# Kernel optimization log

Hardware: AMD Instinct MI355X
Metric: run time of the kernel (lower is better)

Reference implementation:

```python
import jax, jax.numpy as jnp
import numpy as np

N = 30000   # nodes
E = 600000  # edges (avg degree 20)
H = 128     # hidden_channels
L = 4       # num_layers
G = 64      # graphs in batch


def _init(key, shape, fan_in):
    return (jax.random.normal(key, shape, jnp.float32) / np.sqrt(fan_in)).astype(jnp.float32)


def setup_inputs() -> dict:
    key = jax.random.key(0)
    ks = jax.random.split(key, 24)
    x = jax.random.normal(ks[0], (N, 1), jnp.float32)
    pos = jax.random.normal(ks[1], (N, 3), jnp.float32)
    edge_index = jax.random.randint(ks[2], (2, E), 0, N, dtype=jnp.int32).astype(jnp.int64)
    batch = jnp.sort(jax.random.randint(ks[3], (N,), 0, G, dtype=jnp.int32)).astype(jnp.int64)

    emb_w = _init(ks[4], (1, H), 1)
    emb_b = jnp.zeros((H,), jnp.float32)

    # stacked per-layer params: msg MLP (2H+1 -> H -> H), node MLP (2H -> H -> H)
    msg_w1 = _init(ks[5], (L, 2 * H + 1, H), 2 * H + 1)
    msg_b1 = jnp.zeros((L, H), jnp.float32)
    msg_w2 = _init(ks[6], (L, H, H), H)
    msg_b2 = jnp.zeros((L, H), jnp.float32)
    node_w1 = _init(ks[7], (L, 2 * H, H), 2 * H)
    node_b1 = jnp.zeros((L, H), jnp.float32)
    node_w2 = _init(ks[8], (L, H, H), H)
    node_b2 = jnp.zeros((L, H), jnp.float32)

    out_w1 = _init(ks[9], (H, 32), H)
    out_b1 = jnp.zeros((32,), jnp.float32)
    out_w2 = _init(ks[10], (32, 1), 32)
    out_b2 = jnp.zeros((1,), jnp.float32)

    return {
        "x": x, "pos": pos, "edge_index": edge_index, "batch": batch,
        "emb_w": emb_w, "emb_b": emb_b,
        "msg_w1": msg_w1, "msg_b1": msg_b1, "msg_w2": msg_w2, "msg_b2": msg_b2,
        "node_w1": node_w1, "node_b1": node_b1, "node_w2": node_w2, "node_b2": node_b2,
        "out_w1": out_w1, "out_b1": out_b1, "out_w2": out_w2, "out_b2": out_b2,
    }


def reference(x, pos, edge_index, batch,
              emb_w, emb_b,
              msg_w1, msg_b1, msg_w2, msg_b2,
              node_w1, node_b1, node_w2, node_b2,
              out_w1, out_b1, out_w2, out_b2):
    row, col = edge_index[0], edge_index[1]  # row = source j, col = target i
    # edge scalar: squared distance (computed once, reused across layers)
    dist_sq = jnp.sum((pos[row] - pos[col]) ** 2, axis=-1, keepdims=True)  # [E,1]

    h = x @ emb_w + emb_b  # [N,H]
    for l in range(L):
        x_j = h[row]   # source features
        x_i = h[col]   # target features
        m = jnp.concatenate([x_i, x_j, dist_sq], axis=-1)           # [E, 2H+1]
        m = jax.nn.silu(m @ msg_w1[l] + msg_b1[l]) @ msg_w2[l] + msg_b2[l]  # [E,H]
        aggr = jax.ops.segment_sum(m, col, num_segments=N)          # scatter-add to targets
        nh = jnp.concatenate([h, aggr], axis=-1)                    # [N, 2H]
        h = jax.nn.silu(nh @ node_w1[l] + node_b1[l]) @ node_w2[l] + node_b2[l]
        # dropout omitted for deterministic reference (eval mode)

    g = jax.ops.segment_sum(h, batch, num_segments=G)               # global_add_pool [G,H]
    return jax.nn.silu(g @ out_w1 + out_b1) @ out_w2 + out_b2       # [G,1]
```

## Files before the change

kernel.cpp:

```cpp
#include <hip/hip_runtime.h>

typedef unsigned short u16;
typedef __bf16 bf16x8 __attribute__((ext_vector_type(8)));
typedef float f32x4 __attribute__((ext_vector_type(4)));

#define HN 128
#define TM 64
#define LTM 16
#define ASTRIDE 136

__device__ __forceinline__ u16 f2bf(float f) {
  union { float f; unsigned u; } v; v.f = f;
  unsigned r = v.u + 0x7fffu + ((v.u >> 16) & 1u);
  return (u16)(r >> 16);
}
__device__ __forceinline__ float bf2f(u16 v) {
  union { unsigned u; float f; } x; x.u = ((unsigned)v) << 16; return x.f;
}
__device__ __forceinline__ float bflo(unsigned v) {
  union { unsigned u; float f; } x; x.u = v << 16; return x.f;
}
__device__ __forceinline__ float bfhi(unsigned v) {
  union { unsigned u; float f; } x; x.u = v & 0xffff0000u; return x.f;
}
__device__ __forceinline__ float silu_f(float x) {
  float e = __builtin_amdgcn_exp2f(-1.442695041f * x);
  return x * __builtin_amdgcn_rcpf(1.f + e);
}

__global__ void pack_weights(const float* __restrict__ msg_w1, const float* __restrict__ msg_w2,
                             const float* __restrict__ node_w1, const float* __restrict__ node_w2,
                             u16* __restrict__ pw, int* __restrict__ deg,
                             float* __restrict__ g, int N_, int GH) {
  int id = blockIdx.x * 256 + threadIdx.x;
  if (id < N_) deg[id] = 0;
  if (id < GH) g[id] = 0.f;
  if (id >= 4 * 6 * 16384) return;
  int l = id / (6 * 16384);
  int rem = id % (6 * 16384);
  int m = rem / 16384;
  int e = rem % 16384;
  int kg = e >> 10;
  int n = (e >> 3) & 127;
  int j = e & 7;
  int k = kg * 8 + j;
  float v = 0.f;
  switch (m) {
    case 0: v = msg_w1[(l * 257 + k) * 128 + n]; break;
    case 1: v = msg_w1[(l * 257 + 128 + k) * 128 + n]; break;
    case 2: v = msg_w2[(l * 128 + k) * 128 + n]; break;
    case 3: v = node_w1[(l * 256 + k) * 128 + n]; break;
    case 4: v = node_w1[(l * 256 + 128 + k) * 128 + n]; break;
    case 5: v = node_w2[(l * 128 + k) * 128 + n]; break;
  }
  pw[id] = f2bf(v);
}

__device__ __forceinline__ void gemm64(const u16* s_A, const u16* s_W,
                                       int w, int quad, int m16, f32x4 acc[8]) {
#pragma unroll
  for (int ks = 0; ks < 4; ks++) {
    bf16x8 a = *(const bf16x8*)&s_A[(w * 16 + m16) * ASTRIDE + ks * 32 + quad * 8];
#pragma unroll
    for (int ct = 0; ct < 8; ct++) {
      bf16x8 b = *(const bf16x8*)&s_W[(ks * 4 + quad) * 1024 + (ct * 16 + m16) * 8];
      acc[ct] = __builtin_amdgcn_mfma_f32_16x16x32_bf16(a, b, acc[ct], 0, 0, 0);
    }
  }
}

__device__ __forceinline__ void gemm16_gb(const u16* s_A, const u16* __restrict__ gW,
                                          int ch, int quad, int m16, f32x4 acc[2]) {
#pragma unroll
  for (int ks = 0; ks < 4; ks++) {
    bf16x8 a = *(const bf16x8*)&s_A[m16 * ASTRIDE + ks * 32 + quad * 8];
#pragma unroll
    for (int ct = 0; ct < 2; ct++) {
      bf16x8 b = *(const bf16x8*)&gW[(ks * 4 + quad) * 1024 + ((ch * 2 + ct) * 16 + m16) * 8];
      acc[ct] = __builtin_amdgcn_mfma_f32_16x16x32_bf16(a, b, acc[ct], 0, 0, 0);
    }
  }
}

__device__ __forceinline__ void gemm16_ra_gb(const bf16x8 aH[4], const u16* __restrict__ gW,
                                             int ch, int quad, int m16, f32x4 acc[2]) {
#pragma unroll
  for (int ks = 0; ks < 4; ks++) {
#pragma unroll
    for (int ct = 0; ct < 2; ct++) {
      bf16x8 b = *(const bf16x8*)&gW[(ks * 4 + quad) * 1024 + ((ch * 2 + ct) * 16 + m16) * 8];
      acc[ct] = __builtin_amdgcn_mfma_f32_16x16x32_bf16(aH[ks], b, acc[ct], 0, 0, 0);
    }
  }
}

__global__ __launch_bounds__(256) void fold_kernel(
    const float* __restrict__ msg_w2, const float* __restrict__ node_w1,
    const float* __restrict__ msg_b2, const u16* __restrict__ pw,
    u16* __restrict__ pwc, float* __restrict__ vc,
    const float* __restrict__ msg_w1, const float* __restrict__ emb_w,
    const float* __restrict__ emb_b, const float* __restrict__ msg_b1,
    float* __restrict__ uv) {
  __shared__ __align__(16) u16 s_A[TM * ASTRIDE];
  __shared__ __align__(16) u16 s_W[16384];
  const int t = threadIdx.x;
  const int w = t >> 6, lane = t & 63, quad = lane >> 4, m16 = lane & 15;
  const int b = blockIdx.x, l = b >> 1, half = b & 1;
  const int tile0 = half * 64;

  {
    int r = t >> 2, qo = (t & 3) * 32;
    const float4* src = (const float4*)(msg_w2 + (size_t)(l * 128 + tile0 + r) * 128 + qo);
    u16* dst = s_A + r * ASTRIDE + qo;
#pragma unroll
    for (int i = 0; i < 8; i++) {
      float4 v = src[i];
      ushort4 o;
      o.x = f2bf(v.x); o.y = f2bf(v.y); o.z = f2bf(v.z); o.w = f2bf(v.w);
      *(ushort4*)(dst + i * 4) = o;
    }
  }
  {
    const int4* src = (const int4*)(pw + (size_t)(l * 6 + 4) * 16384);
    int4* dst = (int4*)s_W;
#pragma unroll
    for (int i = 0; i < 8; i++) dst[t + i * 256] = src[t + i * 256];
  }
  __syncthreads();
  f32x4 acc[8];
#pragma unroll
  for (int ct = 0; ct < 8; ct++) acc[ct] = {0.f, 0.f, 0.f, 0.f};
  gemm64(s_A, s_W, w, quad, m16, acc);
#pragma unroll
  for (int ct = 0; ct < 8; ct++)
#pragma unroll
    for (int j = 0; j < 4; j++) {
      int k = tile0 + w * 16 + quad * 4 + j;
      int n = ct * 16 + m16;
      pwc[(size_t)l * 16384 + (k >> 3) * 1024 + n * 8 + (k & 7)] = f2bf(acc[ct][j]);
    }
  if (half == 0 && t < 128) {
    float s = 0.f;
    for (int np = 0; np < 128; np++)
      s += msg_b2[l * 128 + np] * node_w1[(size_t)(l * 256 + 128 + np) * 128 + t];
    vc[l * 128 + t] = s;
  }
  if (l == 0 && half == 1 && t < 128) {
    float up = 0.f, vp = 0.f, uq = 0.f, vq = 0.f;
    for (int k = 0; k < 128; k++) {
      float wa = msg_w1[(size_t)k * 128 + t];
      float wb = msg_w1[(size_t)(128 + k) * 128 + t];
      up = fmaf(emb_w[k], wa, up);
      vp = fmaf(emb_b[k], wa, vp);
      uq = fmaf(emb_w[k], wb, uq);
      vq = fmaf(emb_b[k], wb, vq);
    }
    uv[t] = up;
    uv[128 + t] = vp + vq + msg_b1[t];
    uv[256 + t] = uq;
  }
}

__global__ void hist_kernel(const int* __restrict__ eidx, int* __restrict__ deg,
                            int* __restrict__ rnk, int E_) {
  int e = blockIdx.x * 256 + threadIdx.x;
  if (e < E_) rnk[e] = atomicAdd(&deg[eidx[E_ + e]], 1);
}

__global__ void scan1_kernel(const int* __restrict__ deg, int* __restrict__ off,
                             int* __restrict__ bsum, int n) {
  __shared__ int s[256];
  int t = threadIdx.x;
  int i = blockIdx.x * 256 + t;
  int v = (i < n) ? deg[i] : 0;
  s[t] = v;
  for (int d = 1; d < 256; d <<= 1) {
    __syncthreads();
    int x = (t >= d) ? s[t - d] : 0;
    __syncthreads();
    s[t] += x;
  }
  __syncthreads();
  if (i < n) off[i] = s[t] - v;
  if (t == 255) bsum[blockIdx.x] = s[255];
}

__global__ void scan2_kernel(int* __restrict__ bsum, int nb) {
  __shared__ int s[256];
  int t = threadIdx.x;
  int v = (t < nb) ? bsum[t] : 0;
  s[t] = v;
  for (int d = 1; d < 256; d <<= 1) {
    __syncthreads();
    int x = (t >= d) ? s[t - d] : 0;
    __syncthreads();
    s[t] += x;
  }
  __syncthreads();
  if (t < nb) bsum[t] = s[t] - v;
}

__global__ void scan3_kernel(int* __restrict__ off, const int* __restrict__ bsum, int n) {
  int i = blockIdx.x * 256 + threadIdx.x;
  if (i < n) off[i] += bsum[blockIdx.x];
}

__global__ void scatter_kernel(const int* __restrict__ eidx, const float* __restrict__ pos,
                               const int* __restrict__ off, const int* __restrict__ rnk,
                               int2* __restrict__ es8, int E_) {
  int e = blockIdx.x * 256 + threadIdx.x;
  if (e >= E_) return;
  int sr = eidx[e], tg = eidx[E_ + e];
  float dx = pos[sr * 3 + 0] - pos[tg * 3 + 0];
  float dy = pos[sr * 3 + 1] - pos[tg * 3 + 1];
  float dz = pos[sr * 3 + 2] - pos[tg * 3 + 2];
  float d = dx * dx + dy * dy + dz * dz;
  int p = off[tg] + rnk[e];
  int2 v;
  v.x = sr | (tg << 15);
  v.y = __float_as_int(d);
  es8[p] = v;
}

__device__ __forceinline__ void edge_step_lds(
    int tg_s, float dd_s, unsigned qv,
    int& cur_s, float& p0, float& p1, float& s0, float& s1,
    const u16* __restrict__ P, float* s_S, int cp,
    float wd0, float wd1, int tile0) {
  if (tg_s != cur_s) {
    if (cur_s >= 0) {
      float* dst = &s_S[(cur_s - tile0) * HN + cp];
      atomicAdd(dst, s0);
      atomicAdd(dst + 1, s1);
    }
    cur_s = tg_s; s0 = 0.f; s1 = 0.f;
    int cg = tg_s < 0 ? 0 : tg_s;
    unsigned pv = *(const unsigned*)&P[(size_t)cg * HN + cp];
    p0 = bflo(pv); p1 = bfhi(pv);
  }
  float x0 = p0 + bflo(qv) + dd_s * wd0;
  float x1 = p1 + bfhi(qv) + dd_s * wd1;
  s0 += silu_f(x0);
  s1 += silu_f(x1);
}

__device__ __forceinline__ void edge_step_r1(
    int tg_s, float dd_s, float xs,
    int& cur_s, float& p0, float& p1, float& s0, float& s1,
    const float* s_xt, float* s_S, int cp,
    float wd0, float wd1, float uP0, float uP1, float vP0, float vP1,
    float uQ0, float uQ1, int tile0) {
  if (tg_s != cur_s) {
    if (cur_s >= 0) {
      float* dst = &s_S[(cur_s - tile0) * HN + cp];
      atomicAdd(dst, s0);
      atomicAdd(dst + 1, s1);
    }
    cur_s = tg_s; s0 = 0.f; s1 = 0.f;
    int ci = tg_s < 0 ? 0 : (tg_s - tile0);
    float xt = s_xt[ci];
    p0 = fmaf(xt, uP0, vP0);
    p1 = fmaf(xt, uP1, vP1);
  }
  float x0 = fmaf(dd_s, wd0, fmaf(xs, uQ0, p0));
  float x1 = fmaf(dd_s, wd1, fmaf(xs, uQ1, p1));
  s0 += silu_f(x0);
  s1 += silu_f(x1);
}

template <bool FUSE, bool RANK1>
__global__ __launch_bounds__(256) void layer_kernel(
    const u16* __restrict__ P, const u16* __restrict__ Q,
    const u16* __restrict__ hbf, u16* __restrict__ hout,
    const int* __restrict__ off, const int* __restrict__ deg,
    const float* __restrict__ w1d, const int2* __restrict__ es8,
    const u16* __restrict__ pwc, const float* __restrict__ vc,
    const u16* __restrict__ pwn, const float* __restrict__ b1, const float* __restrict__ b2,
    const u16* __restrict__ pw_next, const float* __restrict__ b1_next,
    u16* __restrict__ Pout, u16* __restrict__ Qout,
    const float* __restrict__ xin, const float* __restrict__ uv,
    const float* __restrict__ emb_w, const float* __restrict__ emb_b,
    int nnodes, int E_) {
  __shared__ float s_S[LTM * HN];
  __shared__ __align__(16) u16 s_A[LTM * ASTRIDE];
  __shared__ float s_xt[LTM];
  const int t = threadIdx.x;
  const int w = t >> 6, lane = t & 63, quad = lane >> 4, m16 = lane & 15;
  const int tile0 = blockIdx.x * LTM;
  const int ch = w;

  {
    float4 z = {0.f, 0.f, 0.f, 0.f};
    float4* p4 = (float4*)s_S;
#pragma unroll
    for (int i = 0; i < 2; i++) p4[t + i * 256] = z;
  }
  if constexpr (RANK1) {
    if (t < LTM) {
      int n = tile0 + t;
      s_xt[t] = (n < nnodes) ? xin[n] : 0.f;
    }
  }
  __syncthreads();

  const int cp = lane * 2;
  const float2 wdv = *(const float2*)&w1d[cp];
  const float wd0 = wdv.x, wd1 = wdv.y;
  const int e_lo = off[tile0];
  const int e_hi = (tile0 + LTM < nnodes) ? off[tile0 + LTM] : E_;
  const int span = e_hi - e_lo;
  const int wstart = e_lo + (span * w) / 4;
  const int wend = e_lo + (span * (w + 1)) / 4;
  const int total = wend - wstart;
  const int nchunks = (total + 63) >> 6;

  int cur_s = -1;
  float s0 = 0.f, s1 = 0.f, p0 = 0.f, p1 = 0.f;

  if constexpr (RANK1) {
    __shared__ float s_xs[4][2][64];
    const float uP0 = uv[cp], uP1 = uv[cp + 1];
    const float vP0 = uv[128 + cp], vP1 = uv[128 + cp + 1];
    const float uQ0 = uv[256 + cp], uQ1 = uv[256 + cp + 1];
    if (nchunks > 0) {
      int2* ebuf = (int2*)(s_A + (w * 4) * ASTRIDE);
      float* xsb = &s_xs[w][0][0];
      {
        int e = wstart + lane;
        int2 v;
        if (e < wend) v = es8[e];
        else { v.x = (int)0xFFFF8000; v.y = 0; }
        float xl = xin[v.x & 0x7fff];
        ebuf[lane] = v;
        xsb[lane] = xl;
      }
      asm volatile("s_waitcnt lgkmcnt(0)" ::: "memory");
      int tg[8]; float dd[8]; float xs[8];
#pragma unroll
      for (int j = 0; j < 8; j++) {
        int2 v = ebuf[j];
        tg[j] = v.x >> 15; dd[j] = __int_as_float(v.y);
        xs[j] = xsb[j];
      }

      for (int ci = 0; ci < nchunks; ci++) {
        const int cs = (ci & 1), ns = ((ci + 1) & 1);
        const int2* cb = ebuf + cs * 64;
        const float* cx = xsb + cs * 64;
        const int2* nb = ebuf + ns * 64;
        const float* nx = xsb + ns * 64;
        int2 vnext; vnext.x = (int)0xFFFF8000; vnext.y = 0;
        {
          int e = wstart + (ci + 1) * 64 + lane;
          if (ci + 1 < nchunks && e < wend) vnext = es8[e];
        }
#pragma unroll
        for (int g = 0; g < 3; g++) {
          int tgn[8]; float ddn[8]; float xsn[8];
#pragma unroll
          for (int j = 0; j < 8; j++) {
            int2 v = cb[(g + 1) * 8 + j];
            tgn[j] = v.x >> 15; ddn[j] = __int_as_float(v.y);
            xsn[j] = cx[(g + 1) * 8 + j];
          }
#pragma unroll
          for (int j = 0; j < 8; j++) {
            int tg_s = __builtin_amdgcn_readfirstlane(tg[j]);
            edge_step_r1(tg_s, dd[j], xs[j], cur_s, p0, p1, s0, s1, s_xt, s_S, cp,
                         wd0, wd1, uP0, uP1, vP0, vP1, uQ0, uQ1, tile0);
          }
#pragma unroll
          for (int j = 0; j < 8; j++) { tg[j] = tgn[j]; dd[j] = ddn[j]; xs[j] = xsn[j]; }
        }
        float xnext = xin[vnext.x & 0x7fff];
#pragma unroll
        for (int g = 3; g < 7; g++) {
          int tgn[8]; float ddn[8]; float xsn[8];
#pragma unroll
          for (int j = 0; j < 8; j++) {
            int2 v = cb[(g + 1) * 8 + j];
            tgn[j] = v.x >> 15; ddn[j] = __int_as_float(v.y);
            xsn[j] = cx[(g + 1) * 8 + j];
          }
#pragma unroll
          for (int j = 0; j < 8; j++) {
            int tg_s = __builtin_amdgcn_readfirstlane(tg[j]);
            edge_step_r1(tg_s, dd[j], xs[j], cur_s, p0, p1, s0, s1, s_xt, s_S, cp,
                         wd0, wd1, uP0, uP1, vP0, vP1, uQ0, uQ1, tile0);
          }
#pragma unroll
          for (int j = 0; j < 8; j++) { tg[j] = tgn[j]; dd[j] = ddn[j]; xs[j] = xsn[j]; }
        }
        ebuf[ns * 64 + lane] = vnext;
        xsb[ns * 64 + lane] = xnext;
        asm volatile("s_waitcnt lgkmcnt(0)" ::: "memory");
        {
          int tgn[8]; float ddn[8]; float xsn[8];
#pragma unroll
          for (int j = 0; j < 8; j++) {
            int2 v = nb[j];
            tgn[j] = v.x >> 15; ddn[j] = __int_as_float(v.y);
            xsn[j] = nx[j];
          }
#pragma unroll
          for (int j = 0; j < 8; j++) {
            int tg_s = __builtin_amdgcn_readfirstlane(tg[j]);
            edge_step_r1(tg_s, dd[j], xs[j], cur_s, p0, p1, s0, s1, s_xt, s_S, cp,
                         wd0, wd1, uP0, uP1, vP0, vP1, uQ0, uQ1, tile0);
          }
#pragma unroll
          for (int j = 0; j < 8; j++) { tg[j] = tgn[j]; dd[j] = ddn[j]; xs[j] = xsn[j]; }
        }
      }
      if (cur_s >= 0) {
        float* dst = &s_S[(cur_s - tile0) * HN + cp];
        atomicAdd(dst, s0);
        atomicAdd(dst + 1, s1);
      }
    }
  } else {
    if (nchunks > 0) {
      int2* ebuf = (int2*)(s_A + (w * 4) * ASTRIDE);
      {
        int e = wstart + lane;
        int2 v;
        if (e < wend) v = es8[e];
        else { v.x = (int)0xFFFF8000; v.y = 0; }
        ebuf[lane] = v;
      }
      asm volatile("s_waitcnt lgkmcnt(0)" ::: "memory");
      int tg[8]; float dd[8]; unsigned qv[8];
#pragma unroll
      for (int j = 0; j < 8; j++) {
        int2 v = ebuf[j];
        tg[j] = v.x >> 15; dd[j] = __int_as_float(v.y);
        qv[j] = *(const unsigned*)&Q[(size_t)(v.x & 0x7fff) * HN + cp];
      }

      for (int ci = 0; ci < nchunks; ci++) {
        const int2* cb = ebuf + (ci & 1) * 64;
        const int2* nb = ebuf + ((ci + 1) & 1) * 64;
        int2 vnext; vnext.x = (int)0xFFFF8000; vnext.y = 0;
        {
          int e = wstart + (ci + 1) * 64 + lane;
          if (ci + 1 < nchunks && e < wend) vnext = es8[e];
        }
#pragma unroll
        for (int g = 0; g < 7; g++) {
          int tgn[8]; float ddn[8]; unsigned qvn[8];
#pragma unroll
          for (int j = 0; j < 8; j++) {
            int2 v = cb[(g + 1) * 8 + j];
            tgn[j] = v.x >> 15; ddn[j] = __int_as_float(v.y);
            qvn[j] = *(const unsigned*)&Q[(size_t)(v.x & 0x7fff) * HN + cp];
          }
#pragma unroll
          for (int j = 0; j < 8; j++) {
            int tg_s = __builtin_amdgcn_readfirstlane(tg[j]);
            edge_step_lds(tg_s, dd[j], qv[j], cur_s, p0, p1, s0, s1, P, s_S, cp, wd0, wd1, tile0);
          }
#pragma unroll
          for (int j = 0; j < 8; j++) { tg[j] = tgn[j]; dd[j] = ddn[j]; qv[j] = qvn[j]; }
        }
        ebuf[((ci + 1) & 1) * 64 + lane] = vnext;
        asm volatile("s_waitcnt lgkmcnt(0)" ::: "memory");
        {
          int tgn[8]; float ddn[8]; unsigned qvn[8];
#pragma unroll
          for (int j = 0; j < 8; j++) {
            int2 v = nb[j];
            tgn[j] = v.x >> 15; ddn[j] = __int_as_float(v.y);
            qvn[j] = *(const unsigned*)&Q[(size_t)(v.x & 0x7fff) * HN + cp];
          }
#pragma unroll
          for (int j = 0; j < 8; j++) {
            int tg_s = __builtin_amdgcn_readfirstlane(tg[j]);
            edge_step_lds(tg_s, dd[j], qv[j], cur_s, p0, p1, s0, s1, P, s_S, cp, wd0, wd1, tile0);
          }
#pragma unroll
          for (int j = 0; j < 8; j++) { tg[j] = tgn[j]; dd[j] = ddn[j]; qv[j] = qvn[j]; }
        }
      }
      if (cur_s >= 0) {
        float* dst = &s_S[(cur_s - tile0) * HN + cp];
        atomicAdd(dst, s0);
        atomicAdd(dst + 1, s1);
      }
    }
  }
  __syncthreads();

  {
    int srow = w * 4 + (lane >> 4);
    int scol = (lane & 15) * 8;
    const float4* src = (const float4*)&s_S[srow * HN + scol];
    u16* dst = s_A + srow * ASTRIDE + scol;
    float4 v0 = src[0];
    float4 v1 = src[1];
    ushort4 o0, o1;
    o0.x = f2bf(v0.x); o0.y = f2bf(v0.y); o0.z = f2bf(v0.z); o0.w = f2bf(v0.w);
    o1.x = f2bf(v1.x); o1.y = f2bf(v1.y); o1.z = f2bf(v1.z); o1.w = f2bf(v1.w);
    *(ushort4*)(dst + 0) = o0;
    *(ushort4*)(dst + 4) = o1;
  }
  __syncthreads();

  float bb1[2], vcr[2], bb2[2], bbn[2];
#pragma unroll
  for (int ct = 0; ct < 2; ct++) {
    int c = (ch * 2 + ct) * 16 + m16;
    bb1[ct] = b1[c];
    vcr[ct] = vc[c];
    bb2[ct] = b2[c];
    bbn[ct] = FUSE ? b1_next[c] : 0.f;
  }
  int nodem = tile0 + m16;
  if (nodem >= nnodes) nodem = nnodes - 1;

  f32x4 acc[2];
#pragma unroll
  for (int ct = 0; ct < 2; ct++) acc[ct] = {0.f, 0.f, 0.f, 0.f};
  gemm16_gb(s_A, pwc, ch, quad, m16, acc);

  bf16x8 aH[4];
  if constexpr (RANK1) {
    float xv = s_xt[m16];
#pragma unroll
    for (int ks = 0; ks < 4; ks++) {
      u16 hv[8];
#pragma unroll
      for (int i = 0; i < 8; i++) {
        int c = ks * 32 + quad * 8 + i;
        hv[i] = f2bf(fmaf(xv, emb_w[c], emb_b[c]));
      }
      aH[ks] = *(bf16x8*)hv;
    }
  } else {
#pragma unroll
    for (int ks = 0; ks < 4; ks++)
      aH[ks] = *(const bf16x8*)&hbf[(size_t)nodem * HN + ks * 32 + quad * 8];
  }
  gemm16_ra_gb(aH, pwn, ch, quad, m16, acc);

  {
    float degv[4];
#pragma unroll
    for (int j = 0; j < 4; j++) {
      int n = tile0 + quad * 4 + j;
      if (n >= nnodes) n = nnodes - 1;
      degv[j] = (float)deg[n];
    }
#pragma unroll
    for (int ct = 0; ct < 2; ct++)
#pragma unroll
      for (int j = 0; j < 4; j++) {
        int row = quad * 4 + j;
        float xv = acc[ct][j] + bb1[ct] + degv[j] * vcr[ct];
        s_A[row * ASTRIDE + (ch * 2 + ct) * 16 + m16] = f2bf(silu_f(xv));
      }
  }
  __syncthreads();

#pragma unroll
  for (int ct = 0; ct < 2; ct++) acc[ct] = {0.f, 0.f, 0.f, 0.f};
  gemm16_gb(s_A, pwn + 32768, ch, quad, m16, acc);

#pragma unroll
  for (int ct = 0; ct < 2; ct++)
#pragma unroll
    for (int j = 0; j < 4; j++) {
      int row = quad * 4 + j;
      int n = tile0 + row;
      u16 hv = f2bf(acc[ct][j] + bb2[ct]);
      if (n < nnodes) hout[(size_t)n * HN + (ch * 2 + ct) * 16 + m16] = hv;
      if (FUSE) s_A[row * ASTRIDE + (ch * 2 + ct) * 16 + m16] = hv;
    }

  if (FUSE) {
    __syncthreads();
#pragma unroll
    for (int ct = 0; ct < 2; ct++) acc[ct] = {0.f, 0.f, 0.f, 0.f};
    gemm16_gb(s_A, pw_next, ch, quad, m16, acc);
#pragma unroll
    for (int ct = 0; ct < 2; ct++)
#pragma unroll
      for (int j = 0; j < 4; j++) {
        int n = tile0 + quad * 4 + j;
        if (n < nnodes) Pout[(size_t)n * HN + (ch * 2 + ct) * 16 + m16] = f2bf(acc[ct][j] + bbn[ct]);
      }
#pragma unroll
    for (int ct = 0; ct < 2; ct++) acc[ct] = {0.f, 0.f, 0.f, 0.f};
    gemm16_gb(s_A, pw_next + 16384, ch, quad, m16, acc);
#pragma unroll
    for (int ct = 0; ct < 2; ct++)
#pragma unroll
      for (int j = 0; j < 4; j++) {
        int n = tile0 + quad * 4 + j;
        if (n < nnodes) Qout[(size_t)n * HN + (ch * 2 + ct) * 16 + m16] = f2bf(acc[ct][j]);
      }
  }
}

__global__ __launch_bounds__(256) void pool_kernel(
    const u16* __restrict__ h, const int* __restrict__ batch,
    float* __restrict__ g, int N) {
  __shared__ int s_b[64];
  const int t = threadIdx.x;
  const int n0 = blockIdx.x * 64;
  if (t < 64) {
    int n = n0 + t;
    s_b[t] = (n < N) ? batch[n] : -1;
  }
  __syncthreads();
  const int cp = (t & 63) * 2;
  const int rg = t >> 6;
  int cur = -1;
  float s0 = 0.f, s1 = 0.f;
#pragma unroll 4
  for (int i = 0; i < 16; i++) {
    int r = rg * 16 + i;
    int b = s_b[r];
    if (b < 0) break;
    if (b != cur) {
      if (cur >= 0) {
        atomicAdd(&g[cur * HN + cp], s0);
        atomicAdd(&g[cur * HN + cp + 1], s1);
      }
      cur = b; s0 = 0.f; s1 = 0.f;
    }
    unsigned v = *(const unsigned*)&h[(size_t)(n0 + r) * HN + cp];
    s0 += bf2f((u16)(v & 0xffffu));
    s1 += bf2f((u16)(v >> 16));
  }
  if (cur >= 0) {
    atomicAdd(&g[cur * HN + cp], s0);
    atomicAdd(&g[cur * HN + cp + 1], s1);
  }
}

__global__ __launch_bounds__(64) void out_kernel(
    const float* __restrict__ g, const float* __restrict__ w1,
    const float* __restrict__ b1, const float* __restrict__ w2,
    const float* __restrict__ b2, float* __restrict__ out) {
  const int gi = blockIdx.x;
  const int t = threadIdx.x;
  const int c = t & 31, kh = t >> 5;
  float s = 0.f;
  for (int k = kh * 64; k < kh * 64 + 64; k++)
    s += g[gi * HN + k] * w1[k * 32 + c];
  s += __shfl_down(s, 32);
  float r = 0.f;
  if (kh == 0) r = silu_f(s + b1[c]) * w2[c];
  r += __shfl_down(r, 16);
  r += __shfl_down(r, 8);
  r += __shfl_down(r, 4);
  r += __shfl_down(r, 2);
  r += __shfl_down(r, 1);
  if (t == 0) out[gi] = r + b2[0];
}

extern "C" void kernel_launch(void* const* d_in, const int* in_sizes, int n_in,
                              void* d_out, int out_size, void* d_ws, size_t ws_size,
                              hipStream_t stream) {
  const float* x = (const float*)d_in[0];
  const float* pos = (const float*)d_in[1];
  const int* eidx = (const int*)d_in[2];
  const int* batch = (const int*)d_in[3];
  const float* emb_w = (const float*)d_in[4];
  const float* emb_b = (const float*)d_in[5];
  const float* msg_w1 = (const float*)d_in[6];
  const float* msg_b1 = (const float*)d_in[7];
  const float* msg_w2 = (const float*)d_in[8];
  const float* msg_b2 = (const float*)d_in[9];
  const float* node_w1 = (const float*)d_in[10];
  const float* node_b1 = (const float*)d_in[11];
  const float* node_w2 = (const float*)d_in[12];
  const float* node_b2 = (const float*)d_in[13];
  const float* out_w1 = (const float*)d_in[14];
  const float* out_b1 = (const float*)d_in[15];
  const float* out_w2 = (const float*)d_in[16];
  const float* out_b2 = (const float*)d_in[17];
  float* outp = (float*)d_out;

  const int N = 30000, E = 600000, G = 64;
  const size_t NH = (size_t)N * HN;

  u16* hA = (u16*)d_ws;
  u16* hB = hA + NH;
  u16* Pa = hB + NH;
  u16* Qa = Pa + NH;
  u16* Pb = Qa + NH;
  u16* Qb = Pb + NH;
  int2* es8 = (int2*)(Qb + NH);
  int* deg = (int*)(es8 + E);
  int* off = deg + N;
  int* bsum = off + N;
  float* g = (float*)(bsum + 128);
  u16* pw = (u16*)(g + G * HN);
  u16* pwc = pw + (size_t)4 * 6 * 16384;
  float* vcb = (float*)(pwc + (size_t)4 * 16384);
  float* uvb = vcb + 4 * 128;
  int* rnk = (int*)Pb;

  const int NB = (N + 255) / 256;
  const int NLB = (N + LTM - 1) / LTM;

  pack_weights<<<(4 * 6 * 16384 + 255) / 256, 256, 0, stream>>>(
      msg_w1, msg_w2, node_w1, node_w2, pw, deg, g, N, G * HN);
  fold_kernel<<<8, 256, 0, stream>>>(msg_w2, node_w1, msg_b2, pw, pwc, vcb,
                                     msg_w1, emb_w, emb_b, msg_b1, uvb);

  hist_kernel<<<(E + 255) / 256, 256, 0, stream>>>(eidx, deg, rnk, E);
  scan1_kernel<<<NB, 256, 0, stream>>>(deg, off, bsum, N);
  scan2_kernel<<<1, 256, 0, stream>>>(bsum, NB);
  scan3_kernel<<<NB, 256, 0, stream>>>(off, bsum, N);
  scatter_kernel<<<(E + 255) / 256, 256, 0, stream>>>(eidx, pos, off, rnk, es8, E);


  for (int l = 0; l < 4; l++) {
    const u16* pwl = pw + (size_t)(l * 6) * 16384;
    const float* w1d = msg_w1 + (size_t)(l * 257 + 256) * 128;
    u16* hin = (l & 1) ? hA : hB;
    u16* hot = (l & 1) ? hB : hA;
    u16* Pin = (l & 1) ? Pb : Pa;
    u16* Qin = (l & 1) ? Qb : Qa;
    u16* Pot = (l & 1) ? Pa : Pb;
    u16* Qot = (l & 1) ? Qa : Qb;
    if (l == 0) {
      layer_kernel<true, true><<<NLB, 256, 0, stream>>>(
          Pin, Qin, hin, hot, off, deg, w1d, es8,
          pwc + (size_t)l * 16384, vcb + l * 128,
          pwl + 3 * 16384, node_b1 + l * 128, node_b2 + l * 128,
          pw + (size_t)((l + 1) * 6) * 16384, msg_b1 + (l + 1) * 128, Pot, Qot,
          x, uvb, emb_w, emb_b, N, E);
    } else if (l < 3) {
      layer_kernel<true, false><<<NLB, 256, 0, stream>>>(
          Pin, Qin, hin, hot, off, deg, w1d, es8,
          pwc + (size_t)l * 16384, vcb + l * 128,
          pwl + 3 * 16384, node_b1 + l * 128, node_b2 + l * 128,
          pw + (size_t)((l + 1) * 6) * 16384, msg_b1 + (l + 1) * 128, Pot, Qot,
          x, uvb, emb_w, emb_b, N, E);
    } else {
      layer_kernel<false, false><<<NLB, 256, 0, stream>>>(
          Pin, Qin, hin, hot, off, deg, w1d, es8,
          pwc + (size_t)l * 16384, vcb + l * 128,
          pwl + 3 * 16384, node_b1 + l * 128, node_b2 + l * 128,
          nullptr, nullptr, nullptr, nullptr,
          x, uvb, emb_w, emb_b, N, E);
    }
  }

  pool_kernel<<<(N + 63) / 64, 256, 0, stream>>>(hB, batch, g, N);
  out_kernel<<<G, 64, 0, stream>>>(g, out_w1, out_b1, out_w2, out_b2, outp);
}
```

Before: 411.6 us.

## Double layer-kernel node tile to 32 rows with 512-thread blocks

Raises the per-block node tile from 16 to 32 nodes and doubles block size to 8 waves. Edge ranges are split across 8 waves, and the node-MLP GEMMs assign each wave a 16-row half and a 32-column chunk, so weights fetched from global memory are reused across twice as many rows. Padding edges (negative target) now return early instead of being clamped. Larger blocks halve the grid and may lower occupancy. NLB is not shown changing with LTM, so grid sizing must already derive from it.

```diff
diff --git a/kernel.cpp b/kernel.cpp
--- a/kernel.cpp
+++ b/kernel.cpp
@@ -6,7 +6,7 @@
 
 #define HN 128
 #define TM 64
-#define LTM 16
+#define LTM 32
 #define ASTRIDE 136
 
 __device__ __forceinline__ u16 f2bf(float f) {
@@ -69,11 +69,11 @@
   }
 }
 
-__device__ __forceinline__ void gemm16_gb(const u16* s_A, const u16* __restrict__ gW,
-                                          int ch, int quad, int m16, f32x4 acc[2]) {
+__device__ __forceinline__ void gemm32q_gb(const u16* s_A, const u16* __restrict__ gW,
+                                           int rh, int ch, int quad, int m16, f32x4 acc[2]) {
 #pragma unroll
   for (int ks = 0; ks < 4; ks++) {
-    bf16x8 a = *(const bf16x8*)&s_A[m16 * ASTRIDE + ks * 32 + quad * 8];
+    bf16x8 a = *(const bf16x8*)&s_A[(rh * 16 + m16) * ASTRIDE + ks * 32 + quad * 8];
 #pragma unroll
     for (int ct = 0; ct < 2; ct++) {
       bf16x8 b = *(const bf16x8*)&gW[(ks * 4 + quad) * 1024 + ((ch * 2 + ct) * 16 + m16) * 8];
@@ -82,8 +82,8 @@
   }
 }
 
-__device__ __forceinline__ void gemm16_ra_gb(const bf16x8 aH[4], const u16* __restrict__ gW,
-                                             int ch, int quad, int m16, f32x4 acc[2]) {
+__device__ __forceinline__ void gemm32q_ra_gb(const bf16x8 aH[4], const u16* __restrict__ gW,
+                                              int ch, int quad, int m16, f32x4 acc[2]) {
 #pragma unroll
   for (int ks = 0; ks < 4; ks++) {
 #pragma unroll
@@ -227,6 +227,7 @@
     int& cur_s, float& p0, float& p1, float& s0, float& s1,
     const u16* __restrict__ P, float* s_S, int cp,
     float wd0, float wd1, int tile0) {
+  if (tg_s < 0) return;
   if (tg_s != cur_s) {
     if (cur_s >= 0) {
       float* dst = &s_S[(cur_s - tile0) * HN + cp];
@@ -234,8 +235,7 @@
       atomicAdd(dst + 1, s1);
     }
     cur_s = tg_s; s0 = 0.f; s1 = 0.f;
-    int cg = tg_s < 0 ? 0 : tg_s;
-    unsigned pv = *(const unsigned*)&P[(size_t)cg * HN + cp];
+    unsigned pv = *(const unsigned*)&P[(size_t)tg_s * HN + cp];
     p0 = bflo(pv); p1 = bfhi(pv);
   }
   float x0 = p0 + bflo(qv) + dd_s * wd0;
@@ -250,6 +250,7 @@
     const float* s_xt, float* s_S, int cp,
     float wd0, float wd1, float uP0, float uP1, float vP0, float vP1,
     float uQ0, float uQ1, int tile0) {
+  if (tg_s < 0) return;
   if (tg_s != cur_s) {
     if (cur_s >= 0) {
       float* dst = &s_S[(cur_s - tile0) * HN + cp];
@@ -257,8 +258,7 @@
       atomicAdd(dst + 1, s1);
     }
     cur_s = tg_s; s0 = 0.f; s1 = 0.f;
-    int ci = tg_s < 0 ? 0 : (tg_s - tile0);
-    float xt = s_xt[ci];
+    float xt = s_xt[tg_s - tile0];
     p0 = fmaf(xt, uP0, vP0);
     p1 = fmaf(xt, uP1, vP1);
   }
@@ -269,7 +269,7 @@
 }
 
 template <bool FUSE, bool RANK1>
-__global__ __launch_bounds__(256) void layer_kernel(
+__global__ __launch_bounds__(512) void layer_kernel(
     const u16* __restrict__ P, const u16* __restrict__ Q,
     const u16* __restrict__ hbf, u16* __restrict__ hout,
     const int* __restrict__ off, const int* __restrict__ deg,
@@ -287,13 +287,14 @@
   const int t = threadIdx.x;
   const int w = t >> 6, lane = t & 63, quad = lane >> 4, m16 = lane & 15;
   const int tile0 = blockIdx.x * LTM;
-  const int ch = w;
+  const int rh = w >> 2;
+  const int ch = w & 3;
 
   {
     float4 z = {0.f, 0.f, 0.f, 0.f};
     float4* p4 = (float4*)s_S;
 #pragma unroll
-    for (int i = 0; i < 2; i++) p4[t + i * 256] = z;
+    for (int i = 0; i < 2; i++) p4[t + i * 512] = z;
   }
   if constexpr (RANK1) {
     if (t < LTM) {
@@ -309,8 +310,8 @@
   const int e_lo = off[tile0];
   const int e_hi = (tile0 + LTM < nnodes) ? off[tile0 + LTM] : E_;
   const int span = e_hi - e_lo;
-  const int wstart = e_lo + (span * w) / 4;
-  const int wend = e_lo + (span * (w + 1)) / 4;
+  const int wstart = e_lo + (span * w) / 8;
+  const int wend = e_lo + (span * (w + 1)) / 8;
   const int total = wend - wstart;
   const int nchunks = (total + 63) >> 6;
 
@@ -318,7 +319,7 @@
   float s0 = 0.f, s1 = 0.f, p0 = 0.f, p1 = 0.f;
 
   if constexpr (RANK1) {
-    __shared__ float s_xs[4][2][64];
+    __shared__ float s_xs[8][2][64];
     const float uP0 = uv[cp], uP1 = uv[cp + 1];
     const float vP0 = uv[128 + cp], vP1 = uv[128 + cp + 1];
     const float uQ0 = uv[256 + cp], uQ1 = uv[256 + cp + 1];
@@ -514,17 +515,17 @@
     bb2[ct] = b2[c];
     bbn[ct] = FUSE ? b1_next[c] : 0.f;
   }
-  int nodem = tile0 + m16;
+  int nodem = tile0 + rh * 16 + m16;
   if (nodem >= nnodes) nodem = nnodes - 1;
 
   f32x4 acc[2];
 #pragma unroll
   for (int ct = 0; ct < 2; ct++) acc[ct] = {0.f, 0.f, 0.f, 0.f};
-  gemm16_gb(s_A, pwc, ch, quad, m16, acc);
+  gemm32q_gb(s_A, pwc, rh, ch, quad, m16, acc);
 
   bf16x8 aH[4];
   if constexpr (RANK1) {
-    float xv = s_xt[m16];
+    float xv = s_xt[rh * 16 + m16];
 #pragma unroll
     for (int ks = 0; ks < 4; ks++) {
       u16 hv[8];
@@ -540,13 +541,13 @@
     for (int ks = 0; ks < 4; ks++)
       aH[ks] = *(const bf16x8*)&hbf[(size_t)nodem * HN + ks * 32 + quad * 8];
   }
-  gemm16_ra_gb(aH, pwn, ch, quad, m16, acc);
+  gemm32q_ra_gb(aH, pwn, ch, quad, m16, acc);
 
   {
     float degv[4];
 #pragma unroll
     for (int j = 0; j < 4; j++) {
-      int n = tile0 + quad * 4 + j;
+      int n = tile0 + rh * 16 + quad * 4 + j;
       if (n >= nnodes) n = nnodes - 1;
       degv[j] = (float)deg[n];
     }
@@ -554,7 +555,7 @@
     for (int ct = 0; ct < 2; ct++)
 #pragma unroll
       for (int j = 0; j < 4; j++) {
-        int row = quad * 4 + j;
+        int row = rh * 16 + quad * 4 + j;
         float xv = acc[ct][j] + bb1[ct] + degv[j] * vcr[ct];
         s_A[row * ASTRIDE + (ch * 2 + ct) * 16 + m16] = f2bf(silu_f(xv));
       }
@@ -563,13 +564,13 @@
 
 #pragma unroll
   for (int ct = 0; ct < 2; ct++) acc[ct] = {0.f, 0.f, 0.f, 0.f};
-  gemm16_gb(s_A, pwn + 32768, ch, quad, m16, acc);
+  gemm32q_gb(s_A, pwn + 32768, rh, ch, quad, m16, acc);
 
 #pragma unroll
   for (int ct = 0; ct < 2; ct++)
 #pragma unroll
     for (int j = 0; j < 4; j++) {
-      int row = quad * 4 + j;
+      int row = rh * 16 + quad * 4 + j;
       int n = tile0 + row;
       u16 hv = f2bf(acc[ct][j] + bb2[ct]);
       if (n < nnodes) hout[(size_t)n * HN + (ch * 2 + ct) * 16 + m16] = hv;
@@ -580,22 +581,22 @@
     __syncthreads();
 #pragma unroll
     for (int ct = 0; ct < 2; ct++) acc[ct] = {0.f, 0.f, 0.f, 0.f};
-    gemm16_gb(s_A, pw_next, ch, quad, m16, acc);
+    gemm32q_gb(s_A, pw_next, rh, ch, quad, m16, acc);
 #pragma unroll
     for (int ct = 0; ct < 2; ct++)
 #pragma unroll
       for (int j = 0; j < 4; j++) {
-        int n = tile0 + quad * 4 + j;
+        int n = tile0 + rh * 16 + quad * 4 + j;
         if (n < nnodes) Pout[(size_t)n * HN + (ch * 2 + ct) * 16 + m16] = f2bf(acc[ct][j] + bbn[ct]);
       }
 #pragma unroll
     for (int ct = 0; ct < 2; ct++) acc[ct] = {0.f, 0.f, 0.f, 0.f};
-    gemm16_gb(s_A, pw_next + 16384, ch, quad, m16, acc);
+    gemm32q_gb(s_A, pw_next + 16384, rh, ch, quad, m16, acc);
 #pragma unroll
     for (int ct = 0; ct < 2; ct++)
 #pragma unroll
       for (int j = 0; j < 4; j++) {
-        int n = tile0 + quad * 4 + j;
+        int n = tile0 + rh * 16 + quad * 4 + j;
         if (n < nnodes) Qout[(size_t)n * HN + (ch * 2 + ct) * 16 + m16] = f2bf(acc[ct][j]);
       }
   }
@@ -727,21 +728,21 @@
     u16* Pot = (l & 1) ? Pa : Pb;
     u16* Qot = (l & 1) ? Qa : Qb;
     if (l == 0) {
-      layer_kernel<true, true><<<NLB, 256, 0, stream>>>(
+      layer_kernel<true, true><<<NLB, 512, 0, stream>>>(
           Pin, Qin, hin, hot, off, deg, w1d, es8,
           pwc + (size_t)l * 16384, vcb + l * 128,
           pwl + 3 * 16384, node_b1 + l * 128, node_b2 + l * 128,
           pw + (size_t)((l + 1) * 6) * 16384, msg_b1 + (l + 1) * 128, Pot, Qot,
           x, uvb, emb_w, emb_b, N, E);
     } else if (l < 3) {
-      layer_kernel<true, false><<<NLB, 256, 0, stream>>>(
+      layer_kernel<true, false><<<NLB, 512, 0, stream>>>(
           Pin, Qin, hin, hot, off, deg, w1d, es8,
           pwc + (size_t)l * 16384, vcb + l * 128,
           pwl + 3 * 16384, node_b1 + l * 128, node_b2 + l * 128,
           pw + (size_t)((l + 1) * 6) * 16384, msg_b1 + (l + 1) * 128, Pot, Qot,
           x, uvb, emb_w, emb_b, N, E);
     } else {
-      layer_kernel<false, false><<<NLB, 256, 0, stream>>>(
+      layer_kernel<false, false><<<NLB, 512, 0, stream>>>(
           Pin, Qin, hin, hot, off, deg, w1d, es8,
           pwc + (size_t)l * 16384, vcb + l * 128,
           pwl + 3 * 16384, node_b1 + l * 128, node_b2 + l * 128,
```

Measured after the change: 398.3 us. 1.03x faster.
